# Kernel tuning notes

Measured on AMD Instinct MI355X. Metric: run time of the kernel, lower is better.

Reference implementation:

```python
import jax, jax.numpy as jnp
import numpy as np

COMMITMENT_COST = 0.25

def setup_inputs() -> dict:
    key = jax.random.key(0)
    k1, k2 = jax.random.split(key)
    inputs = jax.random.normal(k1, (16, 256, 64, 64), dtype=jnp.float32)   # [B, C=D, H, W]
    embedding = jax.random.normal(k2, (2048, 256), dtype=jnp.float32)      # [K, D] codebook
    return {"inputs": inputs, "embedding": embedding}

def reference(inputs, embedding):
    K, D = embedding.shape
    x = jnp.transpose(inputs, (0, 2, 3, 1))            # [B, H, W, D]
    flat = x.reshape(-1, D)                            # [N, D]
    distances = (jnp.sum(flat * flat, axis=1, keepdims=True)
                 + jnp.sum(embedding * embedding, axis=1)
                 - 2.0 * flat @ embedding.T)
    idx = jnp.argmin(distances, axis=1)                # [N]
    encodings = jax.nn.one_hot(idx, K, dtype=flat.dtype)  # [N, K]
    quantized = embedding[idx].reshape(x.shape)        # gather == one_hot @ embedding
    # commitment loss (eval mode: only e_latent term, scaled)
    e_latent_loss = jnp.mean((jax.lax.stop_gradient(quantized) - x) ** 2)
    loss = COMMITMENT_COST * e_latent_loss
    # straight-through estimator
    quantized_st = x + jax.lax.stop_gradient(quantized - x)
    avg_probs = jnp.mean(encodings, axis=0)
    perplexity = jnp.exp(-jnp.sum(avg_probs * jnp.log(avg_probs + 1e-10)))
    return (loss,
            jnp.transpose(quantized_st, (0, 3, 1, 2)),  # back to [B, C, H, W]
            perplexity,
            encodings)
```

## Files before the change

### kernel.cpp

```cpp
#include <hip/hip_runtime.h>

#define KCODES  2048
#define DDIM    256

#define OUT_LOSS 0
#define OUT_Q    1
#define OUT_PERP 16777217
#define OUT_ENC  16777218

#define WS_IDX  0
#define WS_E2   1048576
#define WS_CNT  1056768
#define WS_SUM  1064960
#define WS_EHI  2097152

typedef _Float16 f16x8 __attribute__((ext_vector_type(8)));
typedef _Float16 f16x4 __attribute__((ext_vector_type(4)));
typedef float    f32x4 __attribute__((ext_vector_type(4)));
typedef float    f32x2 __attribute__((ext_vector_type(2)));

__device__ __forceinline__ void gld16(const void* g, void* l) {
    __builtin_amdgcn_global_load_lds((const __attribute__((address_space(1))) void*)g,
                                     (__attribute__((address_space(3))) void*)l, 16, 0, 0);
}

#define MERGE2(m1,i1,m2,i2,n1,j1,n2,j2)                                   \
    {                                                                     \
        const bool w_ = ((n1) < (m1)) || ((n1) == (m1) && (j1) < (i1));   \
        const float w1_ = w_ ? (n1) : (m1); const int wi_ = w_ ? (j1) : (i1); \
        const float l1_ = w_ ? (m1) : (n1); const int li_ = w_ ? (i1) : (j1); \
        const float c2_ = w_ ? (n2) : (m2); const int ci_ = w_ ? (j2) : (i2); \
        const bool s_ = ((c2_) < (l1_)) || ((c2_) == (l1_) && (ci_) < (li_)); \
        (m1) = w1_; (i1) = wi_;                                           \
        (m2) = s_ ? c2_ : l1_; (i2) = s_ ? ci_ : li_;                     \
    }

__launch_bounds__(256)
__global__ void k_e2split(const float* __restrict__ emb, _Float16* __restrict__ Ehi,
                          float* __restrict__ e2, int* __restrict__ counts,
                          float* __restrict__ sumsq) {
    const int wave = threadIdx.x >> 6;
    const int lane = threadIdx.x & 63;
    const int k = blockIdx.x * 4 + wave;
    const float4 v = *(const float4*)(emb + k * DDIM + lane * 4);
    f16x4 h;
    h[0] = (_Float16)v.x; h[1] = (_Float16)v.y; h[2] = (_Float16)v.z; h[3] = (_Float16)v.w;
    *(f16x4*)(Ehi + k * DDIM + lane * 4) = h;
    float s = v.x * v.x + v.y * v.y + v.z * v.z + v.w * v.w;
#pragma unroll
    for (int off = 32; off >= 1; off >>= 1) s += __shfl_down(s, off);
    if (lane == 0) e2[k] = s;
    if (blockIdx.x < 8) counts[blockIdx.x * 256 + threadIdx.x] = 0;
    if (blockIdx.x == 8 && threadIdx.x == 0) sumsq[0] = 0.0f;
}

__launch_bounds__(256, 2)
__global__ void k_main(const float* __restrict__ inp, const float* __restrict__ emb,
                       const _Float16* __restrict__ Ehi, const float* __restrict__ e2g,
                       int* __restrict__ idx_g, int* __restrict__ counts,
                       float* __restrict__ sumsq) {
    __shared__ __align__(16) _Float16 A[128 * 256];
    __shared__ __align__(16) _Float16 Bh[128 * 64];

    const int rb  = blockIdx.x;
    const int b   = rb >> 5;
    const int hw0 = (rb & 31) << 7;
    const int n0  = rb << 7;
    const int tid = threadIdx.x;
    const int w = tid >> 6, lane = tid & 63;
    const int lq = lane >> 4, lm = lane & 15;
    const int wr = (w >> 1) * 64, wc = (w & 1) * 64;
    const int r8 = lane >> 3, c8 = lane & 7;
    const int gch = c8 ^ r8;

    const float* base = inp + (size_t)b * 1048576 + hw0;
#pragma unroll 4
    for (int rr = 0; rr < 16; ++rr) {
        const int row = ((rr & 1) << 6) + lane;
        const int cg  = ((rr >> 1) << 2) + w;
        const float* p = base + (size_t)(cg << 3) * 4096 + row;
        float v[8];
#pragma unroll
        for (int j = 0; j < 8; ++j) v[j] = p[(size_t)j * 4096];
        f16x8 h;
#pragma unroll
        for (int j = 0; j < 8; ++j) h[j] = (_Float16)v[j];
        const int q  = cg >> 3;
        const int ch = cg & 7;
        *(f16x8*)&A[row * 256 + q * 64 + ((ch ^ (row & 7)) << 3)] = h;
    }
    __syncthreads();

    const int sw0 = ((lq    ) ^ (lm & 7)) << 3;
    const int sw1 = ((lq ^ 4) ^ (lm & 7)) << 3;

    float V1[4][4], V2[4][4]; int I1[4][4], I2[4][4];
#pragma unroll
    for (int i = 0; i < 4; ++i)
#pragma unroll
        for (int rr = 0; rr < 4; ++rr) {
            V1[i][rr] = 3.402823466e38f; V2[i][rr] = 3.402823466e38f;
            I1[i][rr] = 0x7fffffff;      I2[i][rr] = 0x7fffffff;
        }

#pragma unroll 1
    for (int ct = 0; ct < 16; ++ct) {
        const int c0 = ct * 128;
        float e2v[4];
#pragma unroll
        for (int j = 0; j < 4; ++j) e2v[j] = e2g[c0 + wc + j * 16 + lm];

        f32x4 acc[4][4];
#pragma unroll
        for (int i = 0; i < 4; ++i)
#pragma unroll
            for (int j = 0; j < 4; ++j) acc[i][j] = (f32x4)(0.0f);

#pragma unroll 1
        for (int kt = 0; kt < 4; ++kt) {
            const int d0 = kt * 64;
            __syncthreads();
#pragma unroll
            for (int i = 0; i < 4; ++i) {
                const int Row = i * 32 + w * 8 + r8;
                gld16(Ehi + (size_t)(c0 + Row) * DDIM + d0 + gch * 8, &Bh[(i * 32 + w * 8) * 64]);
            }
            __syncthreads();
#pragma unroll
            for (int s = 0; s < 2; ++s) {
                const int wch = s * 4 + lq;
                const int sw = s ? sw1 : sw0;
                f16x8 af[4], bf[4];
#pragma unroll
                for (int t = 0; t < 4; ++t) {
                    const int Rb = wc + t * 16 + lm;
                    af[t] = *(const f16x8*)&A[(wr + t * 16 + lm) * 256 + d0 + sw];
                    bf[t] = *(const f16x8*)&Bh[Rb * 64 + ((wch ^ (Rb & 7)) << 3)];
                }
#pragma unroll
                for (int i = 0; i < 4; ++i)
#pragma unroll
                    for (int j = 0; j < 4; ++j)
                        acc[i][j] = __builtin_amdgcn_mfma_f32_16x16x32_f16(af[i], bf[j], acc[i][j], 0, 0, 0);
            }
        }

#pragma unroll
        for (int i = 0; i < 4; ++i)
#pragma unroll
            for (int j = 0; j < 4; ++j) {
                const int idx = c0 + wc + j * 16 + lm;
#pragma unroll
                for (int rr = 0; rr < 4; ++rr) {
                    const float dist = fmaf(-2.0f, acc[i][j][rr], e2v[j]);
                    const bool b1 = dist < V1[i][rr];
                    const bool b2 = dist < V2[i][rr];
                    V2[i][rr] = b1 ? V1[i][rr] : (b2 ? dist : V2[i][rr]);
                    I2[i][rr] = b1 ? I1[i][rr] : (b2 ? idx  : I2[i][rr]);
                    V1[i][rr] = b1 ? dist : V1[i][rr];
                    I1[i][rr] = b1 ? idx  : I1[i][rr];
                }
            }
    }

    __syncthreads();
    float4* red  = (float4*)&A[0];
    float*  refp = (float*)&A[4096];
#pragma unroll
    for (int i = 0; i < 4; ++i)
#pragma unroll
        for (int rr = 0; rr < 4; ++rr) {
            float m1 = V1[i][rr]; int i1 = I1[i][rr];
            float m2 = V2[i][rr]; int i2 = I2[i][rr];
#pragma unroll
            for (int off = 1; off < 16; off <<= 1) {
                const float n1 = __shfl_xor(m1, off); const int j1 = __shfl_xor(i1, off);
                const float n2 = __shfl_xor(m2, off); const int j2 = __shfl_xor(i2, off);
                MERGE2(m1, i1, m2, i2, n1, j1, n2, j2);
            }
            if (lm == 0) {
                const int row = wr + i * 16 + lq * 4 + rr;
                red[row * 2 + (w & 1)] = make_float4(m1, __int_as_float(i1),
                                                     m2, __int_as_float(i2));
            }
        }
    __syncthreads();

    {
        const int rg = w & 1, dh = w >> 1;
        const int r  = (rg << 6) + lane;
        const float4 Ac = red[r * 2];
        const float4 Bc = red[r * 2 + 1];
        const int c0i = __float_as_int(Ac.y), c1i = __float_as_int(Ac.w);
        const int c2i = __float_as_int(Bc.y), c3i = __float_as_int(Bc.w);
        const float* xp = base + (size_t)(dh * 128) * 4096 + r;
        const float* p0 = emb + (size_t)c0i * DDIM + dh * 128;
        const float* p1 = emb + (size_t)c1i * DDIM + dh * 128;
        const float* p2 = emb + (size_t)c2i * DDIM + dh * 128;
        const float* p3 = emb + (size_t)c3i * DDIM + dh * 128;
        float s0 = 0.f, s1 = 0.f, s2 = 0.f, s3 = 0.f, s4 = 0.f;
#pragma unroll 8
        for (int dd = 0; dd < 128; ++dd) {
            const float xv = xp[(size_t)dd * 4096];
            s0 = fmaf(xv, p0[dd], s0);
            s1 = fmaf(xv, p1[dd], s1);
            s2 = fmaf(xv, p2[dd], s2);
            s3 = fmaf(xv, p3[dd], s3);
            s4 = fmaf(xv, xv,     s4);
        }
        refp[0 * 256 + w * 64 + lane] = s0;
        refp[1 * 256 + w * 64 + lane] = s1;
        refp[2 * 256 + w * 64 + lane] = s2;
        refp[3 * 256 + w * 64 + lane] = s3;
        refp[4 * 256 + w * 64 + lane] = s4;
    }
    __syncthreads();

    if (tid < 128) {
        const int r = tid;
        const int g = r >> 6, rl = r & 63;
        float S[5];
#pragma unroll
        for (int k = 0; k < 5; ++k)
            S[k] = refp[k * 256 + g * 64 + rl] + refp[k * 256 + (g + 2) * 64 + rl];
        const float4 Ac = red[r * 2];
        const float4 Bc = red[r * 2 + 1];
        const int cid[4] = {__float_as_int(Ac.y), __float_as_int(Ac.w),
                            __float_as_int(Bc.y), __float_as_int(Bc.w)};
        float bv = 3.402823466e38f; int bi = 0; float sb = 0.f, eb = 0.f;
#pragma unroll
        for (int k = 0; k < 4; ++k) {
            const float ev = e2g[cid[k]];
            const float dv = fmaf(-2.0f, S[k], ev);
            if (dv < bv || (dv == bv && cid[k] < bi)) { bv = dv; bi = cid[k]; sb = S[k]; eb = ev; }
        }
        idx_g[n0 + r] = bi;
        atomicAdd(&counts[bi], 1);
        float lr = S[4] - 2.0f * sb + eb;
#pragma unroll
        for (int off = 32; off >= 1; off >>= 1) lr += __shfl_down(lr, off);
        if ((r & 63) == 0) atomicAdd(sumsq, lr);
    }
}

__launch_bounds__(256)
__global__ void k_out(const float* __restrict__ emb, const int* __restrict__ idx_g,
                      float* __restrict__ outQ, float* __restrict__ enc) {
    __shared__ int idxs[64];
    const int blk = blockIdx.x;
    const int b   = blk >> 6;
    const int hw0 = (blk & 63) << 6;
    const int w = threadIdx.x >> 6, lane = threadIdx.x & 63;
    const int n0 = (b << 12) + hw0;

    if (threadIdx.x < 64) idxs[threadIdx.x] = idx_g[n0 + threadIdx.x];
    __syncthreads();

    const int myidx = idxs[lane];
    const float* qp = emb + (size_t)myidx * DDIM + w * 64;
    float* op = outQ + (size_t)b * 1048576 + (size_t)(w * 64) * 4096 + hw0 + lane;
#pragma unroll 8
    for (int dd = 0; dd < 64; ++dd)
        __builtin_nontemporal_store(qp[dd], op + (size_t)dd * 4096);

    f32x2* erow = (f32x2*)enc + (size_t)n0 * 1024;
#pragma unroll 1
    for (int rr = 0; rr < 64; ++rr) {
        const int id = idxs[rr];
        f32x2* rp = erow + (size_t)rr * 1024;
#pragma unroll
        for (int k = 0; k < 4; ++k) {
            const int c2 = k * 256 + threadIdx.x;
            const int ccc = c2 * 2;
            f32x2 v;
            v[0] = (ccc == id) ? 1.0f : 0.0f;
            v[1] = (ccc + 1 == id) ? 1.0f : 0.0f;
            __builtin_nontemporal_store(v, rp + c2);
        }
    }
}

__launch_bounds__(256)
__global__ void k_finalize(const int* __restrict__ counts, const float* __restrict__ sumsq,
                           float* __restrict__ out) {
    __shared__ float red[256];
    const int t = threadIdx.x;
    float s = 0.0f;
    for (int k = t; k < KCODES; k += 256) {
        const float p = (float)counts[k] * (1.0f / 65536.0f);
        s += p * logf(p + 1e-10f);
    }
    red[t] = s;
    __syncthreads();
    for (int off = 128; off >= 1; off >>= 1) {
        if (t < off) red[t] += red[t + off];
        __syncthreads();
    }
    if (t == 0) {
        out[OUT_PERP] = expf(-red[0]);
        out[OUT_LOSS] = 0.25f * sumsq[0] * (1.0f / 16777216.0f);
    }
}

extern "C" void kernel_launch(void* const* d_in, const int* in_sizes, int n_in,
                              void* d_out, int out_size, void* d_ws, size_t ws_size,
                              hipStream_t stream) {
    const float* inp = (const float*)d_in[0];
    const float* emb = (const float*)d_in[1];
    float* out = (float*)d_out;
    char* wsb  = (char*)d_ws;

    int*      idxg   = (int*)(wsb + WS_IDX);
    float*    e2     = (float*)(wsb + WS_E2);
    int*      counts = (int*)(wsb + WS_CNT);
    float*    sumsq  = (float*)(wsb + WS_SUM);
    _Float16* Ehi    = (_Float16*)(wsb + WS_EHI);

    k_e2split <<<512,  256, 0, stream>>>(emb, Ehi, e2, counts, sumsq);
    k_main    <<<512,  256, 0, stream>>>(inp, emb, Ehi, e2, idxg, counts, sumsq);
    k_out     <<<1024, 256, 0, stream>>>(emb, idxg, out + OUT_Q, out + OUT_ENC);
    k_finalize<<<1,    256, 0, stream>>>(counts, sumsq, out);
}
```

Before: 892.6 us.

## Stage input tile in LDS for rerank and transpose quantized output via LDS

The fp32 rerank of the top-4 candidates in k_main now loads the input columns into a padded LDS tile with coalesced reads. Each row is then reduced across 16 lanes using vectorized float4 codebook loads, replacing the old strided per-thread loop in which only half the threads did the tail work. The loss sum is gathered in LDS before a single global atomic. k_out now gathers codebook rows into an LDS buffer with float4 loads and writes the transposed quantized output from there, using 32-row blocks and twice the grid size. This trades extra LDS traffic and syncs for better-coalesced global access.

```diff
diff --git a/kernel.cpp b/kernel.cpp
--- a/kernel.cpp
+++ b/kernel.cpp
@@ -59,8 +59,9 @@
                        const _Float16* __restrict__ Ehi, const float* __restrict__ e2g,
                        int* __restrict__ idx_g, int* __restrict__ counts,
                        float* __restrict__ sumsq) {
-    __shared__ __align__(16) _Float16 A[128 * 256];
-    __shared__ __align__(16) _Float16 Bh[128 * 64];
+    __shared__ __align__(16) char pool[81920];
+    _Float16* A  = (_Float16*)pool;
+    _Float16* Bh = (_Float16*)(pool + 65536);
 
     const int rb  = blockIdx.x;
     const int b   = rb >> 5;
@@ -164,8 +165,9 @@
     }
 
     __syncthreads();
-    float4* red  = (float4*)&A[0];
-    float*  refp = (float*)&A[4096];
+    float4* red  = (float4*)pool;
+    float*  lsum = (float*)(pool + 4096);
+    float*  xf   = (float*)(pool + 8192);
 #pragma unroll
     for (int i = 0; i < 4; ++i)
 #pragma unroll
@@ -184,93 +186,134 @@
                                                      m2, __int_as_float(i2));
             }
         }
-    __syncthreads();
-
-    {
-        const int rg = w & 1, dh = w >> 1;
-        const int r  = (rg << 6) + lane;
-        const float4 Ac = red[r * 2];
-        const float4 Bc = red[r * 2 + 1];
-        const int c0i = __float_as_int(Ac.y), c1i = __float_as_int(Ac.w);
-        const int c2i = __float_as_int(Bc.y), c3i = __float_as_int(Bc.w);
-        const float* xp = base + (size_t)(dh * 128) * 4096 + r;
-        const float* p0 = emb + (size_t)c0i * DDIM + dh * 128;
-        const float* p1 = emb + (size_t)c1i * DDIM + dh * 128;
-        const float* p2 = emb + (size_t)c2i * DDIM + dh * 128;
-        const float* p3 = emb + (size_t)c3i * DDIM + dh * 128;
-        float s0 = 0.f, s1 = 0.f, s2 = 0.f, s3 = 0.f, s4 = 0.f;
+    if (tid == 0) *lsum = 0.f;
+
+    const int g16 = tid >> 4;
+    float Sp[8][4], X2r[8];
+#pragma unroll
+    for (int rr = 0; rr < 8; ++rr) {
+        X2r[rr] = 0.f;
+#pragma unroll
+        for (int c = 0; c < 4; ++c) Sp[rr][c] = 0.f;
+    }
+
+#pragma unroll 1
+    for (int h = 0; h < 2; ++h) {
+        __syncthreads();
 #pragma unroll 8
-        for (int dd = 0; dd < 128; ++dd) {
-            const float xv = xp[(size_t)dd * 4096];
-            s0 = fmaf(xv, p0[dd], s0);
-            s1 = fmaf(xv, p1[dd], s1);
-            s2 = fmaf(xv, p2[dd], s2);
-            s3 = fmaf(xv, p3[dd], s3);
-            s4 = fmaf(xv, xv,     s4);
-        }
-        refp[0 * 256 + w * 64 + lane] = s0;
-        refp[1 * 256 + w * 64 + lane] = s1;
-        refp[2 * 256 + w * 64 + lane] = s2;
-        refp[3 * 256 + w * 64 + lane] = s3;
-        refp[4 * 256 + w * 64 + lane] = s4;
-    }
-    __syncthreads();
-
-    if (tid < 128) {
-        const int r = tid;
-        const int g = r >> 6, rl = r & 63;
-        float S[5];
-#pragma unroll
-        for (int k = 0; k < 5; ++k)
-            S[k] = refp[k * 256 + g * 64 + rl] + refp[k * 256 + (g + 2) * 64 + rl];
+        for (int k2 = 0; k2 < 32; ++k2) {
+            const int dloc = w * 32 + k2;
+            const float* sp = base + (size_t)(h * 128 + dloc) * 4096;
+            xf[dloc * 129 + lane]      = sp[lane];
+            xf[dloc * 129 + 64 + lane] = sp[64 + lane];
+        }
+        __syncthreads();
+#pragma unroll
+        for (int rr = 0; rr < 8; ++rr) {
+            const int r = g16 * 8 + rr;
+            const float4 Ac = red[r * 2];
+            const float4 Bc = red[r * 2 + 1];
+            const int cid[4] = {__float_as_int(Ac.y), __float_as_int(Ac.w),
+                                __float_as_int(Bc.y), __float_as_int(Bc.w)};
+            float x8[8];
+#pragma unroll
+            for (int j = 0; j < 8; ++j) x8[j] = xf[(lm * 8 + j) * 129 + r];
+#pragma unroll
+            for (int j = 0; j < 8; ++j) X2r[rr] = fmaf(x8[j], x8[j], X2r[rr]);
+#pragma unroll
+            for (int c = 0; c < 4; ++c) {
+                const float* ep = emb + (size_t)cid[c] * DDIM + h * 128 + lm * 8;
+                const float4 e0 = *(const float4*)ep;
+                const float4 e1 = *(const float4*)(ep + 4);
+                float s = Sp[rr][c];
+                s = fmaf(x8[0], e0.x, s); s = fmaf(x8[1], e0.y, s);
+                s = fmaf(x8[2], e0.z, s); s = fmaf(x8[3], e0.w, s);
+                s = fmaf(x8[4], e1.x, s); s = fmaf(x8[5], e1.y, s);
+                s = fmaf(x8[6], e1.z, s); s = fmaf(x8[7], e1.w, s);
+                Sp[rr][c] = s;
+            }
+        }
+    }
+
+    float lracc = 0.f;
+#pragma unroll
+    for (int rr = 0; rr < 8; ++rr) {
+        const int r = g16 * 8 + rr;
+        float s0 = Sp[rr][0], s1 = Sp[rr][1], s2 = Sp[rr][2], s3 = Sp[rr][3];
+        float x2v = X2r[rr];
+#pragma unroll
+        for (int off = 1; off < 16; off <<= 1) {
+            s0 += __shfl_xor(s0, off); s1 += __shfl_xor(s1, off);
+            s2 += __shfl_xor(s2, off); s3 += __shfl_xor(s3, off);
+            x2v += __shfl_xor(x2v, off);
+        }
         const float4 Ac = red[r * 2];
         const float4 Bc = red[r * 2 + 1];
         const int cid[4] = {__float_as_int(Ac.y), __float_as_int(Ac.w),
                             __float_as_int(Bc.y), __float_as_int(Bc.w)};
+        const float S4[4] = {s0, s1, s2, s3};
         float bv = 3.402823466e38f; int bi = 0; float sb = 0.f, eb = 0.f;
 #pragma unroll
         for (int k = 0; k < 4; ++k) {
             const float ev = e2g[cid[k]];
-            const float dv = fmaf(-2.0f, S[k], ev);
-            if (dv < bv || (dv == bv && cid[k] < bi)) { bv = dv; bi = cid[k]; sb = S[k]; eb = ev; }
-        }
-        idx_g[n0 + r] = bi;
-        atomicAdd(&counts[bi], 1);
-        float lr = S[4] - 2.0f * sb + eb;
-#pragma unroll
-        for (int off = 32; off >= 1; off >>= 1) lr += __shfl_down(lr, off);
-        if ((r & 63) == 0) atomicAdd(sumsq, lr);
-    }
+            const float dv = fmaf(-2.0f, S4[k], ev);
+            if (dv < bv || (dv == bv && cid[k] < bi)) { bv = dv; bi = cid[k]; sb = S4[k]; eb = ev; }
+        }
+        if (lm == rr) {
+            idx_g[n0 + r] = bi;
+            atomicAdd(&counts[bi], 1);
+            lracc = x2v - 2.0f * sb + eb;
+        }
+    }
+#pragma unroll
+    for (int off = 32; off >= 1; off >>= 1) lracc += __shfl_down(lracc, off);
+    if (lane == 0) atomicAdd(lsum, lracc);
+    __syncthreads();
+    if (tid == 0) atomicAdd(sumsq, *lsum);
 }
 
 __launch_bounds__(256)
 __global__ void k_out(const float* __restrict__ emb, const int* __restrict__ idx_g,
                       float* __restrict__ outQ, float* __restrict__ enc) {
-    __shared__ int idxs[64];
+    __shared__ __align__(16) float Qs[32][260];
+    __shared__ int idxs[32];
     const int blk = blockIdx.x;
-    const int b   = blk >> 6;
-    const int hw0 = (blk & 63) << 6;
-    const int w = threadIdx.x >> 6, lane = threadIdx.x & 63;
+    const int b   = blk >> 7;
+    const int hw0 = (blk & 127) << 5;
+    const int tid = threadIdx.x;
+    const int w = tid >> 6, lane = tid & 63;
+    const int g = tid >> 4, lm = tid & 15;
     const int n0 = (b << 12) + hw0;
 
-    if (threadIdx.x < 64) idxs[threadIdx.x] = idx_g[n0 + threadIdx.x];
-    __syncthreads();
-
-    const int myidx = idxs[lane];
-    const float* qp = emb + (size_t)myidx * DDIM + w * 64;
-    float* op = outQ + (size_t)b * 1048576 + (size_t)(w * 64) * 4096 + hw0 + lane;
+    if (tid < 32) idxs[tid] = idx_g[n0 + tid];
+    __syncthreads();
+
+#pragma unroll
+    for (int rr = 0; rr < 2; ++rr) {
+        const int r = g * 2 + rr;
+        const float* ep = emb + (size_t)idxs[r] * DDIM + lm * 16;
+#pragma unroll
+        for (int j = 0; j < 4; ++j)
+            *(float4*)&Qs[r][lm * 16 + j * 4] = *(const float4*)(ep + j * 4);
+    }
+    __syncthreads();
+
+    float* op = outQ + (size_t)b * 1048576 + hw0;
+    const int dh = lane >> 5, hl = lane & 31;
 #pragma unroll 8
-    for (int dd = 0; dd < 64; ++dd)
-        __builtin_nontemporal_store(qp[dd], op + (size_t)dd * 4096);
+    for (int dd = 0; dd < 32; ++dd) {
+        const int d = w * 64 + dd * 2 + dh;
+        __builtin_nontemporal_store(Qs[hl][d], op + (size_t)d * 4096 + hl);
+    }
 
     f32x2* erow = (f32x2*)enc + (size_t)n0 * 1024;
 #pragma unroll 1
-    for (int rr = 0; rr < 64; ++rr) {
+    for (int rr = 0; rr < 32; ++rr) {
         const int id = idxs[rr];
         f32x2* rp = erow + (size_t)rr * 1024;
 #pragma unroll
         for (int k = 0; k < 4; ++k) {
-            const int c2 = k * 256 + threadIdx.x;
+            const int c2 = k * 256 + tid;
             const int ccc = c2 * 2;
             f32x2 v;
             v[0] = (ccc == id) ? 1.0f : 0.0f;
@@ -318,6 +361,6 @@
 
     k_e2split <<<512,  256, 0, stream>>>(emb, Ehi, e2, counts, sumsq);
     k_main    <<<512,  256, 0, stream>>>(inp, emb, Ehi, e2, idxg, counts, sumsq);
-    k_out     <<<1024, 256, 0, stream>>>(emb, idxg, out + OUT_Q, out + OUT_ENC);
+    k_out     <<<2048, 256, 0, stream>>>(emb, idxg, out + OUT_Q, out + OUT_ENC);
     k_finalize<<<1,    256, 0, stream>>>(counts, sumsq, out);
 }
```

Measured after the change: 858.0 us. -3.9%, faster.
